# Performance work log

Measured on AMD Instinct MI355X. Metric: run time of the kernel, lower is better.

Reference implementation:

```python
import jax, jax.numpy as jnp
import numpy as np

HIDDEN = 1024
HEADS = 16
N, T1, T2 = 2, 2048, 2048


def setup_inputs() -> dict:
    key = jax.random.key(0)
    k1, k2, k3, k4 = jax.random.split(key, 4)
    q = jax.random.normal(k1, (N, T1, HIDDEN), dtype=jnp.float32)
    encoder_k = jax.random.normal(k2, (N, T2, HIDDEN), dtype=jnp.float32)
    encoder_v = jax.random.normal(k3, (N, T2, HIDDEN), dtype=jnp.float32)
    encoder_attention_mask = jnp.zeros((N, 1, T2, T2), dtype=jnp.float32)
    wo_w = jax.random.normal(k4, (HIDDEN, HIDDEN), dtype=jnp.float32) * (1.0 / np.sqrt(HIDDEN))
    wo_b = jnp.zeros((HIDDEN,), dtype=jnp.float32)
    return {"q": q, "encoder_k": encoder_k, "encoder_v": encoder_v,
            "encoder_attention_mask": encoder_attention_mask,
            "wo_w": wo_w, "wo_b": wo_b}


def _split_heads(x):
    # [N, T, E] -> [N, h, T, d]
    n, t, e = x.shape
    return x.reshape(n, t, HEADS, e // HEADS).transpose(0, 2, 1, 3)


def reference(q, encoder_k, encoder_v, encoder_attention_mask, wo_w, wo_b):
    qh = _split_heads(q)            # [N,h,T1,d]
    kh = _split_heads(encoder_k)    # [N,h,T2,d]
    vh = _split_heads(encoder_v)    # [N,h,T2,d]
    # NOTE: original applies no 1/sqrt(d) scaling
    scores = jnp.einsum('bhqd,bhkd->bhqk', qh, kh) + encoder_attention_mask
    weights = jax.nn.softmax(scores, axis=-1)
    ctx = jnp.einsum('bhqk,bhkd->bhqd', weights, vh)   # [N,h,T1,d]
    ctx = ctx.transpose(0, 2, 1, 3).reshape(q.shape[0], q.shape[1], -1)  # [N,T1,E]
    # wo: Linear (torch: x @ W.T + b) followed by ReLU
    return jax.nn.relu(ctx @ wo_w.T + wo_b)
```

## Files before the change

kernel.cpp:

```cpp
#include <hip/hip_runtime.h>
#include <hip/hip_bf16.h>


typedef short short8 __attribute__((ext_vector_type(8)));
typedef short short4v __attribute__((ext_vector_type(4)));
typedef float floatx4 __attribute__((ext_vector_type(4)));

#define HIDDEN 1024
#define HEADS 16
#define NB 2
#define T1 2048
#define T2 2048

#define LOG2E 1.44269504f
#define SHIFT 28.8539004f
#define VS 68

__device__ __forceinline__ unsigned short f2bf(float f) {
    unsigned u = __float_as_uint(f);
    return (unsigned short)((u + 0x7fffu + ((u >> 16) & 1u)) >> 16);
}

__device__ __forceinline__ short f2bf_native(float f) {
    __hip_bfloat16 h = __float2bfloat16(f);
    return __builtin_bit_cast(short, h);
}

__global__ void zero_kernel(unsigned* f) {
    if (threadIdx.x == 0) *f = 0u;
}

__global__ void prep_kernel(const float4* __restrict__ ek, const float4* __restrict__ ev,
                            const float4* __restrict__ ww, const float4* __restrict__ mask,
                            ushort4* __restrict__ dst, unsigned* __restrict__ flag) {
    const int NK = NB * T2 * HIDDEN / 4;
    const int NW = HIDDEN * HIDDEN / 4;
    if (blockIdx.y == 0) {
        int i = blockIdx.x * blockDim.x + threadIdx.x;
        int stride = gridDim.x * blockDim.x;
        const int n = 2 * NK + NW;
        for (; i < n; i += stride) {
            float4 v = (i < NK) ? ek[i] : (i < 2 * NK) ? ev[i - NK] : ww[i - 2 * NK];
            ushort4 o;
            o.x = f2bf(v.x); o.y = f2bf(v.y); o.z = f2bf(v.z); o.w = f2bf(v.w);
            dst[i] = o;
        }
    } else {
        const int NM = NB * T2 * T2 / 4;
        int i = blockIdx.x * blockDim.x + threadIdx.x;
        int stride = gridDim.x * blockDim.x;
        float mx = 0.f;
        for (; i < NM; i += stride) {
            float4 v = mask[i];
            mx = fmaxf(mx, fmaxf(fmaxf(fabsf(v.x), fabsf(v.y)), fmaxf(fabsf(v.z), fabsf(v.w))));
        }
        for (int d = 32; d; d >>= 1) mx = fmaxf(mx, __shfl_xor(mx, d));
        if ((threadIdx.x & 63) == 0 && mx > 0.f) atomicMax(flag, __float_as_uint(mx));
    }
}

__device__ __forceinline__ void stage_v(short* __restrict__ buf, const short* __restrict__ Vb,
                                        int b, int h, int kc, int tid) {
#pragma unroll
    for (int it = 0; it < 2; ++it) {
        int i = tid + (it << 8);
        int key = i & 63, dg = i >> 6;
        short8 s = *(const short8*)&Vb[(((b * T2) + kc + key) << 10) + (h << 6) + (dg << 3)];
#pragma unroll
        for (int j = 0; j < 8; ++j) buf[(dg * 8 + j) * VS + key] = s[j];
    }
}

__global__ __launch_bounds__(256, 2) void attn_kernel(
        const float* __restrict__ q,
        const short* __restrict__ Kb,
        const short* __restrict__ Vb,
        const float* __restrict__ mask,
        const unsigned* __restrict__ flagp,
        short* __restrict__ ctx)
{
    __shared__ short lV[2][64 * VS];

    const int tid = threadIdx.x;
    const int wave = tid >> 6;
    const int lane = tid & 63;
    const int quad = lane >> 4;
    const int l16 = lane & 15;

    const int b = blockIdx.z;
    const int h = blockIdx.y;
    const int q0 = blockIdx.x * 128;

    const bool use_mask = (*flagp != 0u);

    short8 qf[2][2];
#pragma unroll
    for (int rb = 0; rb < 2; ++rb) {
#pragma unroll
        for (int ks = 0; ks < 2; ++ks) {
            const float* qp = q + (((b * T1) + q0 + wave * 32 + rb * 16 + l16) << 10)
                                + (h << 6) + ks * 32 + quad * 8;
            float4 v0 = *(const float4*)qp;
            float4 v1 = *(const float4*)(qp + 4);
            short8 s;
            s[0] = (short)f2bf(v0.x * LOG2E); s[1] = (short)f2bf(v0.y * LOG2E);
            s[2] = (short)f2bf(v0.z * LOG2E); s[3] = (short)f2bf(v0.w * LOG2E);
            s[4] = (short)f2bf(v1.x * LOG2E); s[5] = (short)f2bf(v1.y * LOG2E);
            s[6] = (short)f2bf(v1.z * LOG2E); s[7] = (short)f2bf(v1.w * LOG2E);
            qf[rb][ks] = s;
        }
    }

    floatx4 o_acc[2][4];
#pragma unroll
    for (int rb = 0; rb < 2; ++rb)
#pragma unroll
        for (int cb = 0; cb < 4; ++cb) o_acc[rb][cb] = (floatx4){0.f, 0.f, 0.f, 0.f};
    float l_st[2] = {0.f, 0.f};

    stage_v(lV[0], Vb, b, h, 0, tid);
    short8 kfrag[4][2];
#pragma unroll
    for (int kb = 0; kb < 4; ++kb)
#pragma unroll
        for (int ks = 0; ks < 2; ++ks)
            kfrag[kb][ks] = *(const short8*)
                &Kb[(((b * T2) + kb * 16 + l16) << 10) + (h << 6) + ks * 32 + quad * 8];
    __syncthreads();

    for (int ic = 0; ic < T2 / 64; ++ic) {
        const int kc = ic << 6;
        const short* cur = lV[ic & 1];
        const bool has_next = (ic + 1 < T2 / 64);
        const int kcn = has_next ? kc + 64 : kc;

        short8 vreg[2];
#pragma unroll
        for (int it = 0; it < 2; ++it) {
            int i = tid + (it << 8);
            int key = i & 63, dg = i >> 6;
            vreg[it] = *(const short8*)&Vb[(((b * T2) + kcn + key) << 10) + (h << 6) + (dg << 3)];
        }

        short8 knext[4][2];
#pragma unroll
        for (int kb = 0; kb < 4; ++kb)
#pragma unroll
            for (int ks = 0; ks < 2; ++ks)
                knext[kb][ks] = *(const short8*)
                    &Kb[(((b * T2) + kcn + kb * 16 + l16) << 10) + (h << 6) + ks * 32 + quad * 8];

        short4v vfrag[4][4];
#pragma unroll
        for (int kb = 0; kb < 4; ++kb)
#pragma unroll
            for (int cb = 0; cb < 4; ++cb)
                vfrag[kb][cb] = *(const short4v*)&cur[(cb * 16 + l16) * VS + kb * 16 + quad * 4];

#pragma unroll
        for (int rb = 0; rb < 2; ++rb) {
            floatx4 st[4];
#pragma unroll
            for (int kb = 0; kb < 4; ++kb) {
                floatx4 a = (floatx4){0.f, 0.f, 0.f, 0.f};
                a = __builtin_amdgcn_mfma_f32_16x16x32_bf16(kfrag[kb][0], qf[rb][0], a, 0, 0, 0);
                a = __builtin_amdgcn_mfma_f32_16x16x32_bf16(kfrag[kb][1], qf[rb][1], a, 0, 0, 0);
                st[kb] = a;
            }
            if (use_mask) {
                int qrow = q0 + wave * 32 + rb * 16 + l16;
#pragma unroll
                for (int kb = 0; kb < 4; ++kb)
#pragma unroll
                    for (int r = 0; r < 4; ++r) {
                        int key = kc + kb * 16 + quad * 4 + r;
                        st[kb][r] += mask[(b * T2 + qrow) * T2 + key] * LOG2E;
                    }
            }
            float rs = 0.f;
            short4v pf[4];
#pragma unroll
            for (int kb = 0; kb < 4; ++kb) {
                float p0 = exp2f(st[kb][0] - SHIFT);
                float p1 = exp2f(st[kb][1] - SHIFT);
                float p2 = exp2f(st[kb][2] - SHIFT);
                float p3 = exp2f(st[kb][3] - SHIFT);
                rs += (p0 + p1) + (p2 + p3);
                pf[kb][0] = f2bf_native(p0);
                pf[kb][1] = f2bf_native(p1);
                pf[kb][2] = f2bf_native(p2);
                pf[kb][3] = f2bf_native(p3);
            }
            rs += __shfl_xor(rs, 16);
            rs += __shfl_xor(rs, 32);
            l_st[rb] += rs;

#pragma unroll
            for (int kb = 0; kb < 4; ++kb)
#pragma unroll
                for (int cb = 0; cb < 4; ++cb)
                    o_acc[rb][cb] = __builtin_amdgcn_mfma_f32_16x16x16bf16_1k(
                        vfrag[kb][cb], pf[kb], o_acc[rb][cb], 0, 0, 0);
        }

        if (has_next) {
            short* nbuf = lV[(ic + 1) & 1];
#pragma unroll
            for (int it = 0; it < 2; ++it) {
                int i = tid + (it << 8);
                int key = i & 63, dg = i >> 6;
#pragma unroll
                for (int j = 0; j < 8; ++j) nbuf[(dg * 8 + j) * VS + key] = vreg[it][j];
            }
        }

#pragma unroll
        for (int kb = 0; kb < 4; ++kb)
#pragma unroll
            for (int ks = 0; ks < 2; ++ks)
                kfrag[kb][ks] = knext[kb][ks];

        __syncthreads();
    }

#pragma unroll
    for (int rb = 0; rb < 2; ++rb) {
        float rinv = 1.0f / l_st[rb];
        int qrow = q0 + wave * 32 + rb * 16 + l16;
#pragma unroll
        for (int cb = 0; cb < 4; ++cb) {
            short4v o;
#pragma unroll
            for (int r = 0; r < 4; ++r) o[r] = (short)f2bf(o_acc[rb][cb][r] * rinv);
            *(short4v*)&ctx[((b * T1 + qrow) << 10) + (h << 6) + cb * 16 + quad * 4] = o;
        }
    }
}

__global__ __launch_bounds__(512) void proj_kernel(
        const short* __restrict__ Cb,
        const short* __restrict__ Wb,
        const float* __restrict__ bias,
        float* __restrict__ out)
{
    __shared__ short lA[2][64 * 72];
    __shared__ short lB[2][128 * 72];

    const int tid = threadIdx.x;
    const int wave = tid >> 6;
    const int lane = tid & 63;
    const int quad = lane >> 4;
    const int l16 = lane & 15;
    const int wm = wave >> 2, wn = wave & 3;
    const int bm = blockIdx.x, bn = blockIdx.y;

    floatx4 acc[2][2];
#pragma unroll
    for (int i = 0; i < 2; ++i)
#pragma unroll
        for (int j = 0; j < 2; ++j) acc[i][j] = (floatx4){0.f, 0.f, 0.f, 0.f};

    short8 ra, rbw[2];
    {
        int row = tid >> 3, c = tid & 7;
        ra = *(const short8*)&Cb[((bm * 64 + row) << 10) + c * 8];
#pragma unroll
        for (int it = 0; it < 2; ++it) {
            int i = tid + it * 512;
            int brow = i >> 3, bc = i & 7;
            rbw[it] = *(const short8*)&Wb[((bn * 128 + brow) << 10) + bc * 8];
        }
    }
    {
        int row = tid >> 3, c = tid & 7;
        *(short8*)&lA[0][row * 72 + c * 8] = ra;
#pragma unroll
        for (int it = 0; it < 2; ++it) {
            int i = tid + it * 512;
            int brow = i >> 3, bc = i & 7;
            *(short8*)&lB[0][brow * 72 + bc * 8] = rbw[it];
        }
    }
    __syncthreads();

    int cur = 0;
    for (int kt = 0; kt < 1024; kt += 64) {
        const bool has_next = (kt + 64 < 1024);
        if (has_next) {
            int row = tid >> 3, c = tid & 7;
            ra = *(const short8*)&Cb[((bm * 64 + row) << 10) + kt + 64 + c * 8];
#pragma unroll
            for (int it = 0; it < 2; ++it) {
                int i = tid + it * 512;
                int brow = i >> 3, bc = i & 7;
                rbw[it] = *(const short8*)&Wb[((bn * 128 + brow) << 10) + kt + 64 + bc * 8];
            }
        }

#pragma unroll
        for (int ks = 0; ks < 2; ++ks) {
            short8 af[2], bf[2];
#pragma unroll
            for (int i = 0; i < 2; ++i)
                af[i] = *(const short8*)&lA[cur][(wm * 32 + i * 16 + l16) * 72 + ks * 32 + quad * 8];
#pragma unroll
            for (int j = 0; j < 2; ++j)
                bf[j] = *(const short8*)&lB[cur][(wn * 32 + j * 16 + l16) * 72 + ks * 32 + quad * 8];
#pragma unroll
            for (int i = 0; i < 2; ++i)
#pragma unroll
                for (int j = 0; j < 2; ++j)
                    acc[i][j] = __builtin_amdgcn_mfma_f32_16x16x32_bf16(af[i], bf[j], acc[i][j], 0, 0, 0);
        }

        if (has_next) {
            int row = tid >> 3, c = tid & 7;
            *(short8*)&lA[cur ^ 1][row * 72 + c * 8] = ra;
#pragma unroll
            for (int it = 0; it < 2; ++it) {
                int i = tid + it * 512;
                int brow = i >> 3, bc = i & 7;
                *(short8*)&lB[cur ^ 1][brow * 72 + bc * 8] = rbw[it];
            }
        }
        __syncthreads();
        cur ^= 1;
    }

    float bv[2];
#pragma unroll
    for (int j = 0; j < 2; ++j) bv[j] = bias[bn * 128 + wn * 32 + j * 16 + l16];

#pragma unroll
    for (int i = 0; i < 2; ++i)
#pragma unroll
        for (int j = 0; j < 2; ++j)
#pragma unroll
            for (int r = 0; r < 4; ++r) {
                int row = bm * 64 + wm * 32 + i * 16 + quad * 4 + r;
                int col = bn * 128 + wn * 32 + j * 16 + l16;
                float v = acc[i][j][r] + bv[j];
                out[(row << 10) + col] = fmaxf(v, 0.f);
            }
}

extern "C" void kernel_launch(void* const* d_in, const int* in_sizes, int n_in,
                              void* d_out, int out_size, void* d_ws, size_t ws_size,
                              hipStream_t stream) {
    const float* q    = (const float*)d_in[0];
    const float* ek   = (const float*)d_in[1];
    const float* ev   = (const float*)d_in[2];
    const float* mask = (const float*)d_in[3];
    const float* wo_w = (const float*)d_in[4];
    const float* wo_b = (const float*)d_in[5];
    float* out = (float*)d_out;

    char* ws = (char*)d_ws;
    unsigned* flag = (unsigned*)ws;
    short* Kb = (short*)(ws + 4096);
    short* Vb = Kb + (NB * T2 * HIDDEN);
    short* Wb = Vb + (NB * T2 * HIDDEN);
    short* Cb = Wb + (HIDDEN * HIDDEN);

    zero_kernel<<<1, 64, 0, stream>>>(flag);
    prep_kernel<<<dim3(512, 2), 256, 0, stream>>>(
        (const float4*)ek, (const float4*)ev, (const float4*)wo_w, (const float4*)mask,
        (ushort4*)Kb, flag);
    attn_kernel<<<dim3(T1 / 128, HEADS, NB), 256, 0, stream>>>(q, Kb, Vb, mask, flag, Cb);
    proj_kernel<<<dim3(64, 8), 512, 0, stream>>>(Cb, Wb, wo_b, out);
}
```

Before: 228.0 us.

## Process two 64-key V tiles per barrier with 128-key staging

Restructures the attention key loop to cover 128 keys per iteration: two 64-key V tiles are staged into LDS per stage, and K fragments for the second half are prefetched mid-iteration. This halves the number of __syncthreads barriers and gives the global V loads more time to complete in flight. In exchange, LDS use doubles (four V buffers) and register pressure rises with four V prefetch registers, which could lower occupancy under launch_bounds(256,2).

```diff
diff --git a/kernel.cpp b/kernel.cpp
--- a/kernel.cpp
+++ b/kernel.cpp
@@ -79,7 +79,7 @@
         const unsigned* __restrict__ flagp,
         short* __restrict__ ctx)
 {
-    __shared__ short lV[2][64 * VS];
+    __shared__ short lV[2][2][64 * VS];
 
     const int tid = threadIdx.x;
     const int wave = tid >> 6;
@@ -118,7 +118,8 @@
         for (int cb = 0; cb < 4; ++cb) o_acc[rb][cb] = (floatx4){0.f, 0.f, 0.f, 0.f};
     float l_st[2] = {0.f, 0.f};
 
-    stage_v(lV[0], Vb, b, h, 0, tid);
+    stage_v(lV[0][0], Vb, b, h, 0, tid);
+    stage_v(lV[0][1], Vb, b, h, 64, tid);
     short8 kfrag[4][2];
 #pragma unroll
     for (int kb = 0; kb < 4; ++kb)
@@ -128,21 +129,92 @@
                 &Kb[(((b * T2) + kb * 16 + l16) << 10) + (h << 6) + ks * 32 + quad * 8];
     __syncthreads();
 
-    for (int ic = 0; ic < T2 / 64; ++ic) {
-        const int kc = ic << 6;
-        const short* cur = lV[ic & 1];
-        const bool has_next = (ic + 1 < T2 / 64);
-        const int kcn = has_next ? kc + 64 : kc;
-
-        short8 vreg[2];
-#pragma unroll
-        for (int it = 0; it < 2; ++it) {
-            int i = tid + (it << 8);
+    for (int icc = 0; icc < T2 / 128; ++icc) {
+        const int kc0 = icc << 7;
+        const bool has_next = (icc + 1 < T2 / 128);
+        const int kcn = has_next ? kc0 + 128 : kc0;
+
+        short8 vreg[4];
+#pragma unroll
+        for (int it = 0; it < 4; ++it) {
+            int i = tid + ((it & 1) << 8);
             int key = i & 63, dg = i >> 6;
-            vreg[it] = *(const short8*)&Vb[(((b * T2) + kcn + key) << 10) + (h << 6) + (dg << 3)];
+            int half = it >> 1;
+            vreg[it] = *(const short8*)
+                &Vb[(((b * T2) + kcn + half * 64 + key) << 10) + (h << 6) + (dg << 3)];
         }
 
         short8 knext[4][2];
+#pragma unroll
+        for (int kb = 0; kb < 4; ++kb)
+#pragma unroll
+            for (int ks = 0; ks < 2; ++ks)
+                knext[kb][ks] = *(const short8*)
+                    &Kb[(((b * T2) + kc0 + 64 + kb * 16 + l16) << 10) + (h << 6) + ks * 32 + quad * 8];
+
+        {
+            const short* cur = lV[icc & 1][0];
+            const int kc = kc0;
+            short4v vfrag[4][4];
+#pragma unroll
+            for (int kb = 0; kb < 4; ++kb)
+#pragma unroll
+                for (int cb = 0; cb < 4; ++cb)
+                    vfrag[kb][cb] = *(const short4v*)&cur[(cb * 16 + l16) * VS + kb * 16 + quad * 4];
+
+#pragma unroll
+            for (int rb = 0; rb < 2; ++rb) {
+                floatx4 st[4];
+#pragma unroll
+                for (int kb = 0; kb < 4; ++kb) {
+                    floatx4 a = (floatx4){0.f, 0.f, 0.f, 0.f};
+                    a = __builtin_amdgcn_mfma_f32_16x16x32_bf16(kfrag[kb][0], qf[rb][0], a, 0, 0, 0);
+                    a = __builtin_amdgcn_mfma_f32_16x16x32_bf16(kfrag[kb][1], qf[rb][1], a, 0, 0, 0);
+                    st[kb] = a;
+                }
+                if (use_mask) {
+                    int qrow = q0 + wave * 32 + rb * 16 + l16;
+#pragma unroll
+                    for (int kb = 0; kb < 4; ++kb)
+#pragma unroll
+                        for (int r = 0; r < 4; ++r) {
+                            int key = kc + kb * 16 + quad * 4 + r;
+                            st[kb][r] += mask[(b * T2 + qrow) * T2 + key] * LOG2E;
+                        }
+                }
+                float rs = 0.f;
+                short4v pf[4];
+#pragma unroll
+                for (int kb = 0; kb < 4; ++kb) {
+                    float p0 = exp2f(st[kb][0] - SHIFT);
+                    float p1 = exp2f(st[kb][1] - SHIFT);
+                    float p2 = exp2f(st[kb][2] - SHIFT);
+                    float p3 = exp2f(st[kb][3] - SHIFT);
+                    rs += (p0 + p1) + (p2 + p3);
+                    pf[kb][0] = f2bf_native(p0);
+                    pf[kb][1] = f2bf_native(p1);
+                    pf[kb][2] = f2bf_native(p2);
+                    pf[kb][3] = f2bf_native(p3);
+                }
+                rs += __shfl_xor(rs, 16);
+                rs += __shfl_xor(rs, 32);
+                l_st[rb] += rs;
+
+#pragma unroll
+                for (int kb = 0; kb < 4; ++kb)
+#pragma unroll
+                    for (int cb = 0; cb < 4; ++cb)
+                        o_acc[rb][cb] = __builtin_amdgcn_mfma_f32_16x16x16bf16_1k(
+                            vfrag[kb][cb], pf[kb], o_acc[rb][cb], 0, 0, 0);
+            }
+        }
+
+#pragma unroll
+        for (int kb = 0; kb < 4; ++kb)
+#pragma unroll
+            for (int ks = 0; ks < 2; ++ks)
+                kfrag[kb][ks] = knext[kb][ks];
+
 #pragma unroll
         for (int kb = 0; kb < 4; ++kb)
 #pragma unroll
@@ -150,67 +222,60 @@
                 knext[kb][ks] = *(const short8*)
                     &Kb[(((b * T2) + kcn + kb * 16 + l16) << 10) + (h << 6) + ks * 32 + quad * 8];
 
-        short4v vfrag[4][4];
-#pragma unroll
-        for (int kb = 0; kb < 4; ++kb)
-#pragma unroll
-            for (int cb = 0; cb < 4; ++cb)
-                vfrag[kb][cb] = *(const short4v*)&cur[(cb * 16 + l16) * VS + kb * 16 + quad * 4];
-
-#pragma unroll
-        for (int rb = 0; rb < 2; ++rb) {
-            floatx4 st[4];
-#pragma unroll
-            for (int kb = 0; kb < 4; ++kb) {
-                floatx4 a = (floatx4){0.f, 0.f, 0.f, 0.f};
-                a = __builtin_amdgcn_mfma_f32_16x16x32_bf16(kfrag[kb][0], qf[rb][0], a, 0, 0, 0);
-                a = __builtin_amdgcn_mfma_f32_16x16x32_bf16(kfrag[kb][1], qf[rb][1], a, 0, 0, 0);
-                st[kb] = a;
-            }
-            if (use_mask) {
-                int qrow = q0 + wave * 32 + rb * 16 + l16;
+        {
+            const short* cur = lV[icc & 1][1];
+            const int kc = kc0 + 64;
+            short4v vfrag[4][4];
+#pragma unroll
+            for (int kb = 0; kb < 4; ++kb)
+#pragma unroll
+                for (int cb = 0; cb < 4; ++cb)
+                    vfrag[kb][cb] = *(const short4v*)&cur[(cb * 16 + l16) * VS + kb * 16 + quad * 4];
+
+#pragma unroll
+            for (int rb = 0; rb < 2; ++rb) {
+                floatx4 st[4];
+#pragma unroll
+                for (int kb = 0; kb < 4; ++kb) {
+                    floatx4 a = (floatx4){0.f, 0.f, 0.f, 0.f};
+                    a = __builtin_amdgcn_mfma_f32_16x16x32_bf16(kfrag[kb][0], qf[rb][0], a, 0, 0, 0);
+                    a = __builtin_amdgcn_mfma_f32_16x16x32_bf16(kfrag[kb][1], qf[rb][1], a, 0, 0, 0);
+                    st[kb] = a;
+                }
+                if (use_mask) {
+                    int qrow = q0 + wave * 32 + rb * 16 + l16;
+#pragma unroll
+                    for (int kb = 0; kb < 4; ++kb)
+#pragma unroll
+                        for (int r = 0; r < 4; ++r) {
+                            int key = kc + kb * 16 + quad * 4 + r;
+                            st[kb][r] += mask[(b * T2 + qrow) * T2 + key] * LOG2E;
+                        }
+                }
+                float rs = 0.f;
+                short4v pf[4];
+#pragma unroll
+                for (int kb = 0; kb < 4; ++kb) {
+                    float p0 = exp2f(st[kb][0] - SHIFT);
+                    float p1 = exp2f(st[kb][1] - SHIFT);
+                    float p2 = exp2f(st[kb][2] - SHIFT);
+                    float p3 = exp2f(st[kb][3] - SHIFT);
+                    rs += (p0 + p1) + (p2 + p3);
+                    pf[kb][0] = f2bf_native(p0);
+                    pf[kb][1] = f2bf_native(p1);
+                    pf[kb][2] = f2bf_native(p2);
+                    pf[kb][3] = f2bf_native(p3);
+                }
+                rs += __shfl_xor(rs, 16);
+                rs += __shfl_xor(rs, 32);
+                l_st[rb] += rs;
+
 #pragma unroll
                 for (int kb = 0; kb < 4; ++kb)
 #pragma unroll
-                    for (int r = 0; r < 4; ++r) {
-                        int key = kc + kb * 16 + quad * 4 + r;
-                        st[kb][r] += mask[(b * T2 + qrow) * T2 + key] * LOG2E;
-                    }
-            }
-            float rs = 0.f;
-            short4v pf[4];
-#pragma unroll
-            for (int kb = 0; kb < 4; ++kb) {
-                float p0 = exp2f(st[kb][0] - SHIFT);
-                float p1 = exp2f(st[kb][1] - SHIFT);
-                float p2 = exp2f(st[kb][2] - SHIFT);
-                float p3 = exp2f(st[kb][3] - SHIFT);
-                rs += (p0 + p1) + (p2 + p3);
-                pf[kb][0] = f2bf_native(p0);
-                pf[kb][1] = f2bf_native(p1);
-                pf[kb][2] = f2bf_native(p2);
-                pf[kb][3] = f2bf_native(p3);
-            }
-            rs += __shfl_xor(rs, 16);
-            rs += __shfl_xor(rs, 32);
-            l_st[rb] += rs;
-
-#pragma unroll
-            for (int kb = 0; kb < 4; ++kb)
-#pragma unroll
-                for (int cb = 0; cb < 4; ++cb)
-                    o_acc[rb][cb] = __builtin_amdgcn_mfma_f32_16x16x16bf16_1k(
-                        vfrag[kb][cb], pf[kb], o_acc[rb][cb], 0, 0, 0);
-        }
-
-        if (has_next) {
-            short* nbuf = lV[(ic + 1) & 1];
-#pragma unroll
-            for (int it = 0; it < 2; ++it) {
-                int i = tid + (it << 8);
-                int key = i & 63, dg = i >> 6;
-#pragma unroll
-                for (int j = 0; j < 8; ++j) nbuf[(dg * 8 + j) * VS + key] = vreg[it][j];
+                    for (int cb = 0; cb < 4; ++cb)
+                        o_acc[rb][cb] = __builtin_amdgcn_mfma_f32_16x16x16bf16_1k(
+                            vfrag[kb][cb], pf[kb], o_acc[rb][cb], 0, 0, 0);
             }
         }
 
@@ -220,6 +285,16 @@
             for (int ks = 0; ks < 2; ++ks)
                 kfrag[kb][ks] = knext[kb][ks];
 
+        if (has_next) {
+#pragma unroll
+            for (int it = 0; it < 4; ++it) {
+                int i = tid + ((it & 1) << 8);
+                int key = i & 63, dg = i >> 6;
+                short* nbuf = lV[(icc + 1) & 1][it >> 1];
+#pragma unroll
+                for (int j = 0; j < 8; ++j) nbuf[(dg * 8 + j) * VS + key] = vreg[it][j];
+            }
+        }
         __syncthreads();
     }
 
```

Result: slower. 233.8 us (+2.5%).
